# Performance work log

Measured on AMD Instinct MI355X. Metric: run time of the kernel, lower is better.

Reference implementation:

```python
import jax, jax.numpy as jnp
import numpy as np

N = 100000
E = 1600000
D = 128  # in_dim == hidden_dim


def _glorot(key, shape):
    lim = np.sqrt(6.0 / (shape[0] + shape[1]))
    return jax.random.uniform(key, shape, jnp.float32, -lim, lim)


def setup_inputs() -> dict:
    key = jax.random.key(0)
    ks = jax.random.split(key, 10)
    x = jax.random.normal(ks[0], (N, D), jnp.float32)
    edge_index = jax.random.randint(ks[1], (2, E), 0, N, jnp.int64)
    return {
        "x": x,
        "edge_index": edge_index,
        "W1": _glorot(ks[2], (D, D)), "b1": jnp.zeros((D,), jnp.float32),
        "W2": _glorot(ks[3], (D, D)), "b2": jnp.zeros((D,), jnp.float32),
        "Wv": _glorot(ks[4], (D, D)), "bv": jnp.zeros((D,), jnp.float32),
        "Wt": _glorot(ks[5], (D, D)), "bt": jnp.zeros((D,), jnp.float32),
    }


def _gcn_conv(x, W, b, src, dst, dis):
    """GCNConv: x' = D^-1/2 (A+I) D^-1/2 (x W) + b (symmetric norm, self-loops)."""
    xw = x @ W  # [N, H]
    coef = dis[src] * dis[dst]  # [E]
    msg = xw[src] * coef[:, None]  # [E, H] gathered messages
    agg = jax.ops.segment_sum(msg, dst, num_segments=x.shape[0])
    agg = agg + (dis * dis)[:, None] * xw  # self-loop contribution
    return agg + b


def reference(x, edge_index, W1, b1, W2, b2, Wv, bv, Wt, bt):
    src, dst = edge_index[0], edge_index[1]
    n = x.shape[0]
    # degree including self-loop; rsqrt normalization
    deg = jax.ops.segment_sum(jnp.ones_like(dst, dtype=x.dtype), dst, num_segments=n) + 1.0
    dis = jax.lax.rsqrt(deg)
    h = jax.nn.relu(_gcn_conv(x, W1, b1, src, dst, dis))  # dropout: eval no-op
    h = _gcn_conv(h, W2, b2, src, dst, dis)  # last layer: no relu
    x_vision = jax.nn.relu(h @ Wv + bv)
    x_text = jax.nn.relu(h @ Wt + bt)
    return (h, x_vision, x_text)
```

## Files before the change

### kernel.cpp

```cpp
#include <hip/hip_runtime.h>
#include <hip/hip_bf16.h>
#include <hip/hip_fp16.h>

#define NODES 100000
#define EDGES 1600000
#define DIM   128

typedef __bf16   bf16x8 __attribute__((ext_vector_type(8)));
typedef float    f32x4  __attribute__((ext_vector_type(4)));
typedef _Float16 f16x8  __attribute__((ext_vector_type(8)));

__device__ __forceinline__ void gather16(const void* gp, void* lp) {
    __builtin_amdgcn_global_load_lds(
        (const __attribute__((address_space(1))) void*)gp,
        (__attribute__((address_space(3))) void*)lp, 16, 0, 0);
}

__device__ __forceinline__ int wave_detect_m64(const void* ei) {
    const unsigned int* u = (const unsigned int*)ei;
    const unsigned long long nz = __ballot(u[2 * (threadIdx.x & 63) + 1] != 0);
    return (nz == 0ULL) ? 1 : 0;
}

__device__ __forceinline__ int load_idx(const void* ei, long long pos, int m64) {
    return m64 ? (int)((const long long*)ei)[pos] : ((const int*)ei)[pos];
}

__global__ __launch_bounds__(256) void init_kernel(
    int* __restrict__ deg, int n, int gn,
    const float* __restrict__ Wa, const float* __restrict__ Wb,
    const float* __restrict__ Wc, const float* __restrict__ Wd,
    __bf16* __restrict__ wfout)
{
    const int bid = blockIdx.x;
    if (bid < gn) {
        const int i = bid * 256 + threadIdx.x;
        if (i < n) deg[i] = 0;
    } else {
        const int pb = bid - gn;
        const int m  = pb >> 6;
        const int d  = (pb & 63) * 256 + threadIdx.x;
        const float* W = (m == 0) ? Wa : (m == 1) ? Wb : (m == 2) ? Wc : Wd;
        const int j  = d & 7;
        const int l  = (d >> 3) & 15;
        const int q  = (d >> 7) & 3;
        const int kt = (d >> 9) & 3;
        const int ct = (d >> 11) & 7;
        wfout[m * 16384 + d] = (__bf16)W[(kt * 32 + q * 8 + j) * DIM + ct * 16 + l];
    }
}

template <int RELU_BIAS, int ABF16, int OUTF16>
__device__ __forceinline__ void gemm_body(
    const void* __restrict__ Ain, const __bf16* __restrict__ Wf,
    const float* __restrict__ bias, void* __restrict__ outp, int M, int bid)
{
    const int wave = threadIdx.x >> 6;
    const int lane = threadIdx.x & 63;
    const int l15  = lane & 15;
    const int quad = lane >> 4;

    const int row0 = bid * 128 + wave * 32;
    if (row0 >= M) return;

    bf16x8 afA[4], afB[4];
#pragma unroll
    for (int t = 0; t < 2; t++) {
        const int arow  = row0 + t * 16 + l15;
        const int arowc = arow < M ? arow : (M - 1);
        bf16x8* af = t ? afB : afA;
        if (ABF16) {
            const __bf16* ap = (const __bf16*)Ain + (size_t)arowc * DIM + quad * 8;
#pragma unroll
            for (int kt = 0; kt < 4; kt++) af[kt] = *(const bf16x8*)(ap + kt * 32);
        } else {
            const float* ap = (const float*)Ain + (size_t)arowc * DIM + quad * 8;
#pragma unroll
            for (int kt = 0; kt < 4; kt++) {
                const f32x4 lo = *(const f32x4*)(ap + kt * 32);
                const f32x4 hi = *(const f32x4*)(ap + kt * 32 + 4);
                bf16x8 r;
#pragma unroll
                for (int j = 0; j < 4; j++) { r[j] = (__bf16)lo[j]; r[j + 4] = (__bf16)hi[j]; }
                af[kt] = r;
            }
        }
    }

#pragma unroll
    for (int ct = 0; ct < 8; ct++) {
        f32x4 cA = {0.f, 0.f, 0.f, 0.f};
        f32x4 cB = {0.f, 0.f, 0.f, 0.f};
#pragma unroll
        for (int kt = 0; kt < 4; kt++) {
            const bf16x8 b = *(const bf16x8*)(Wf + (ct * 4 + kt) * 512 + lane * 8);
            cA = __builtin_amdgcn_mfma_f32_16x16x32_bf16(afA[kt], b, cA, 0, 0, 0);
            cB = __builtin_amdgcn_mfma_f32_16x16x32_bf16(afB[kt], b, cB, 0, 0, 0);
        }
        const float bb = RELU_BIAS ? bias[ct * 16 + l15] : 0.f;
#pragma unroll
        for (int t = 0; t < 2; t++) {
            const f32x4 c = t ? cB : cA;
#pragma unroll
            for (int r = 0; r < 4; r++) {
                const int row = row0 + t * 16 + quad * 4 + r;
                if (row < M) {
                    float v = c[r];
                    if (RELU_BIAS) { v += bb; v = v > 0.f ? v : 0.f; }
                    const size_t idx = (size_t)row * DIM + ct * 16 + l15;
                    if (OUTF16) ((_Float16*)outp)[idx] = (_Float16)v;
                    else        ((float*)outp)[idx]    = v;
                }
            }
        }
    }
}

template <int RELU_BIAS, int ABF16, int OUTF16>
__global__ __launch_bounds__(256) void gemm128_kernel(
    const void* __restrict__ Ain, const __bf16* __restrict__ Wf,
    const float* __restrict__ bias, void* __restrict__ outp, int M)
{
    gemm_body<RELU_BIAS, ABF16, OUTF16>(Ain, Wf, bias, outp, M, blockIdx.x);
}

__global__ __launch_bounds__(256) void gemm1_count_kernel(
    const float* __restrict__ x, const __bf16* __restrict__ wf1,
    _Float16* __restrict__ xwh, int M, int gm,
    const void* __restrict__ ei, int* __restrict__ deg, int e_cnt)
{
    const int bid = blockIdx.x;
    if (bid < gm) {
        gemm_body<0, 0, 1>(x, wf1, nullptr, xwh, M, bid);
    } else {
        const int m64 = wave_detect_m64(ei);
        const int i = (bid - gm) * 256 + threadIdx.x;
        if (i < e_cnt) atomicAdd(&deg[load_idx(ei, (long long)EDGES + i, m64)], 1);
    }
}

__global__ __launch_bounds__(256) void gemm128_dual_kernel(
    const float* __restrict__ A,
    const __bf16* __restrict__ Wf1, const float* __restrict__ b1,
    const __bf16* __restrict__ Wf2, const float* __restrict__ b2,
    float* __restrict__ out1, float* __restrict__ out2, int M)
{
    const int wave = threadIdx.x >> 6;
    const int lane = threadIdx.x & 63;
    const int l15  = lane & 15;
    const int quad = lane >> 4;

    const int row0 = blockIdx.x * 128 + wave * 32;
    if (row0 >= M) return;

    bf16x8 afA[4], afB[4];
#pragma unroll
    for (int t = 0; t < 2; t++) {
        const int arow  = row0 + t * 16 + l15;
        const int arowc = arow < M ? arow : (M - 1);
        const float* ap = A + (size_t)arowc * DIM + quad * 8;
        bf16x8* af = t ? afB : afA;
#pragma unroll
        for (int kt = 0; kt < 4; kt++) {
            const f32x4 lo = *(const f32x4*)(ap + kt * 32);
            const f32x4 hi = *(const f32x4*)(ap + kt * 32 + 4);
            bf16x8 r;
#pragma unroll
            for (int j = 0; j < 4; j++) { r[j] = (__bf16)lo[j]; r[j + 4] = (__bf16)hi[j]; }
            af[kt] = r;
        }
    }

#pragma unroll
    for (int ct = 0; ct < 8; ct++) {
        f32x4 cA1 = {0.f,0.f,0.f,0.f}, cA2 = {0.f,0.f,0.f,0.f};
        f32x4 cB1 = {0.f,0.f,0.f,0.f}, cB2 = {0.f,0.f,0.f,0.f};
#pragma unroll
        for (int kt = 0; kt < 4; kt++) {
            const bf16x8 w1 = *(const bf16x8*)(Wf1 + (ct * 4 + kt) * 512 + lane * 8);
            const bf16x8 w2 = *(const bf16x8*)(Wf2 + (ct * 4 + kt) * 512 + lane * 8);
            cA1 = __builtin_amdgcn_mfma_f32_16x16x32_bf16(afA[kt], w1, cA1, 0, 0, 0);
            cA2 = __builtin_amdgcn_mfma_f32_16x16x32_bf16(afA[kt], w2, cA2, 0, 0, 0);
            cB1 = __builtin_amdgcn_mfma_f32_16x16x32_bf16(afB[kt], w1, cB1, 0, 0, 0);
            cB2 = __builtin_amdgcn_mfma_f32_16x16x32_bf16(afB[kt], w2, cB2, 0, 0, 0);
        }
        const float bb1 = b1[ct * 16 + l15];
        const float bb2 = b2[ct * 16 + l15];
#pragma unroll
        for (int t = 0; t < 2; t++) {
            const f32x4 c1 = t ? cB1 : cA1;
            const f32x4 c2 = t ? cB2 : cA2;
#pragma unroll
            for (int r = 0; r < 4; r++) {
                const int row = row0 + t * 16 + quad * 4 + r;
                if (row < M) {
                    float v1 = c1[r] + bb1; v1 = v1 > 0.f ? v1 : 0.f;
                    float v2 = c2[r] + bb2; v2 = v2 > 0.f ? v2 : 0.f;
                    out1[(size_t)row * DIM + ct * 16 + l15] = v1;
                    out2[(size_t)row * DIM + ct * 16 + l15] = v2;
                }
            }
        }
    }
}

__global__ __launch_bounds__(256) void scan1_kernel(const int* __restrict__ deg,
                                                    int* __restrict__ offs,
                                                    int* __restrict__ bsum,
                                                    float* __restrict__ dis, int n) {
    __shared__ int sm[256];
    const int t = threadIdx.x, i = blockIdx.x * 256 + t;
    const int v = (i < n) ? deg[i] : 0;
    sm[t] = v;
    __syncthreads();
    for (int d = 1; d < 256; d <<= 1) {
        const int add = (t >= d) ? sm[t - d] : 0;
        __syncthreads();
        sm[t] += add;
        __syncthreads();
    }
    if (i < n) {
        offs[i] = sm[t] - v;
        dis[i]  = rsqrtf((float)v + 1.0f);
    }
    if (t == 255) bsum[blockIdx.x] = sm[255];
}

__global__ __launch_bounds__(256) void scan23_kernel(int* __restrict__ offs,
                                                     const int* __restrict__ bsum,
                                                     int* __restrict__ cursor, int n) {
    __shared__ int sm[256];
    const int t = threadIdx.x, bid = blockIdx.x;
    int part = 0;
    for (int j = t; j < bid; j += 256) part += bsum[j];
    sm[t] = part;
    __syncthreads();
    for (int d = 128; d > 0; d >>= 1) {
        if (t < d) sm[t] += sm[t + d];
        __syncthreads();
    }
    const int boff = sm[0];
    const int i = bid * 256 + t;
    if (i < n) {
        const int o = offs[i] + boff;
        offs[i]   = o;
        cursor[i] = o;
    }
    if (bid == 0 && t == 0) offs[n] = EDGES;
}

__global__ __launch_bounds__(256) void fill_csr_kernel(const void* __restrict__ ei,
                                                       const float* __restrict__ dis,
                                                       int* __restrict__ cursor,
                                                       int2* __restrict__ csr,
                                                       int e_cnt) {
    const int m64 = wave_detect_m64(ei);
    const int e = blockIdx.x * 256 + threadIdx.x;
    if (e >= e_cnt) return;
    const int s = load_idx(ei, e, m64);
    const int d = load_idx(ei, (long long)EDGES + e, m64);
    const int idx = atomicAdd(&cursor[d], 1);
    int2 rec;
    rec.x = s;
    rec.y = __float_as_int(dis[s] * dis[d]);
    csr[idx] = rec;
}

template <int RELU, int WF32, int WBF16>
__global__ __launch_bounds__(256) void aggregate_kernel(
    const int* __restrict__ offs, const int2* __restrict__ csr,
    const float* __restrict__ dis, const _Float16* __restrict__ xw,
    const float* __restrict__ bias, float* __restrict__ out_f32,
    __bf16* __restrict__ out_bf, int n)
{
    __shared__ _Float16 sbuf[4][2][8 * DIM];
    const int wid  = threadIdx.x >> 6;
    const int v    = blockIdx.x * 4 + wid;
    const int lane = threadIdx.x & 63;
    const int l15  = lane & 15;
    const int seg  = lane >> 4;
    const int lmod = lane & 7;

    const int beg = offs[v];
    const int deg = offs[v + 1] - beg;
    const int nb  = (deg + 7) >> 3;
    int lim = beg + deg - 1; if (lim < 0) lim = 0;

    _Float16* bufA = &sbuf[wid][0][0];
    _Float16* bufB = &sbuf[wid][1][0];

    f32x4 a0 = {0.f,0.f,0.f,0.f}, a1 = {0.f,0.f,0.f,0.f};
    if (seg == 0) {
        const float dv = dis[v];
        const float s2 = dv * dv;
        const f16x8 xv = *(const f16x8*)(xw + (size_t)v * DIM + l15 * 8);
#pragma unroll
        for (int j = 0; j < 4; j++) {
            a0[j] += s2 * (float)xv[j];
            a1[j] += s2 * (float)xv[j + 4];
        }
    }

    int p0 = beg + lmod;            p0 = p0 < lim ? p0 : lim;
    int2 rc = csr[p0];
#pragma unroll
    for (int g = 0; g < 2; g++) {
        const int rs = __shfl(rc.x, g * 4 + seg);
        gather16(xw + (size_t)rs * DIM + l15 * 8, bufA + g * 512);
    }
    int p1 = beg + 8 + lmod;        p1 = p1 < lim ? p1 : lim;
    int2 rn1 = csr[p1];
    int p2 = beg + 16 + lmod;       p2 = p2 < lim ? p2 : lim;
    int2 rn2 = csr[p2];

    for (int b = 0; b < nb; ++b) {
        _Float16*       nbuf = (b & 1) ? bufA : bufB;
        const _Float16* cbuf = (b & 1) ? bufB : bufA;
        const bool more = (b + 1 < nb);
        int2 rn3 = rn2;

        if (more) {
#pragma unroll
            for (int g = 0; g < 2; g++) {
                const int rs = __shfl(rn1.x, g * 4 + seg);
                gather16(xw + (size_t)rs * DIM + l15 * 8, nbuf + g * 512);
            }
            __builtin_amdgcn_sched_barrier(0);
            int p3 = beg + (b + 3) * 8 + lmod;  p3 = p3 < lim ? p3 : lim;
            rn3 = csr[p3];
            __builtin_amdgcn_sched_barrier(0);
            asm volatile("s_waitcnt vmcnt(3)" ::: "memory");
            __builtin_amdgcn_sched_barrier(0);
        } else {
            asm volatile("s_waitcnt vmcnt(0)" ::: "memory");
            __builtin_amdgcn_sched_barrier(0);
        }

        const float cfy = __int_as_float(rc.y);
        const int rem = deg - b * 8;
#pragma unroll
        for (int s = 0; s < 2; s++) {
            const int r = s * 4 + seg;
            const float cr = __shfl(cfy, r);
            if (r < rem) {
                const f16x8 hv = *(const f16x8*)(cbuf + s * 512 + lane * 8);
#pragma unroll
                for (int j = 0; j < 4; j++) {
                    a0[j] += cr * (float)hv[j];
                    a1[j] += cr * (float)hv[j + 4];
                }
            }
        }
        rc = rn1; rn1 = rn2; rn2 = rn3;
    }

#pragma unroll
    for (int j = 0; j < 4; j++) {
        a0[j] += __shfl_xor(a0[j], 16); a0[j] += __shfl_xor(a0[j], 32);
        a1[j] += __shfl_xor(a1[j], 16); a1[j] += __shfl_xor(a1[j], 32);
    }

    if (seg == 0) {
        const int cc = l15 * 8;
#pragma unroll
        for (int j = 0; j < 4; j++) { a0[j] += bias[cc + j]; a1[j] += bias[cc + 4 + j]; }
        if (RELU) {
#pragma unroll
            for (int j = 0; j < 4; j++) {
                a0[j] = a0[j] > 0.f ? a0[j] : 0.f;
                a1[j] = a1[j] > 0.f ? a1[j] : 0.f;
            }
        }
        if (WF32) {
            *(f32x4*)(out_f32 + (size_t)v * DIM + cc)     = a0;
            *(f32x4*)(out_f32 + (size_t)v * DIM + cc + 4) = a1;
        }
        if (WBF16) {
            bf16x8 bv;
#pragma unroll
            for (int j = 0; j < 4; j++) { bv[j] = (__bf16)a0[j]; bv[j + 4] = (__bf16)a1[j]; }
            *(bf16x8*)(out_bf + (size_t)v * DIM + cc) = bv;
        }
    }
    asm volatile("s_waitcnt vmcnt(0)" ::: "memory");
}

extern "C" void kernel_launch(void* const* d_in, const int* in_sizes, int n_in,
                              void* d_out, int out_size, void* d_ws, size_t ws_size,
                              hipStream_t stream)
{
    const int N = NODES, E = EDGES;
    const size_t ND = (size_t)N * DIM;

    const float* x  = (const float*)d_in[0];
    const void*  ei = d_in[1];
    const float* W1 = (const float*)d_in[2];
    const float* b1 = (const float*)d_in[3];
    const float* W2 = (const float*)d_in[4];
    const float* b2 = (const float*)d_in[5];
    const float* Wv = (const float*)d_in[6];
    const float* bv = (const float*)d_in[7];
    const float* Wt = (const float*)d_in[8];
    const float* bt = (const float*)d_in[9];

    char* w = (char*)d_ws;
    int*    deg    = (int*)(w + (1 << 10));
    float*  dis    = (float*)(w + (512 << 10));
    int*    offs   = (int*)(w + (1 << 20));
    int*    cursor = (int*)(w + 1572864);
    int*    bsum   = (int*)(w + 2097152);
    int2*   csr    = (int2*)(w + 3145728);
    __bf16* wf     = (__bf16*)(w + 16000000);
    __bf16* wf1 = wf, *wf2 = wf + 16384, *wfv = wf + 32768, *wft = wf + 49152;

    float* out   = (float*)d_out;
    float* slot0 = out;
    float* slot1 = out + ND;
    float* slot2 = out + 2 * ND;
    __bf16*   h1bf = (__bf16*)slot1;
    _Float16* xwh  = (_Float16*)slot2;

    const int GN   = (N + 255) / 256;
    const int GE   = (E + 255) / 256;
    const int GM   = (N + 127) / 128;
    const int GAG  = (N + 3) / 4;

    init_kernel<<<GN + 256, 256, 0, stream>>>(deg, N, GN, W1, W2, Wv, Wt, wf);
    gemm1_count_kernel<<<GM + GE, 256, 0, stream>>>(x, wf1, xwh, N, GM, ei, deg, E);
    scan1_kernel<<<GN, 256, 0, stream>>>(deg, offs, bsum, dis, N);
    scan23_kernel<<<GN, 256, 0, stream>>>(offs, bsum, cursor, N);
    fill_csr_kernel<<<GE, 256, 0, stream>>>(ei, dis, cursor, csr, E);

    aggregate_kernel<1, 0, 1><<<GAG, 256, 0, stream>>>(offs, csr, dis, xwh, b1,
                                                       nullptr, h1bf, N);
    gemm128_kernel<0, 1, 1><<<GM, 256, 0, stream>>>(h1bf, wf2, nullptr, xwh, N);
    aggregate_kernel<0, 1, 0><<<GAG, 256, 0, stream>>>(offs, csr, dis, xwh, b2,
                                                       slot0, nullptr, N);
    gemm128_dual_kernel<<<GM, 256, 0, stream>>>(slot0, wfv, bv, wft, bt, slot1, slot2, N);
}
```

Baseline: 517.5 us.

## Build CSR with two-pass bucketed scatter instead of per-edge global atomics

Replaces the single fill_csr pass, which did one global atomic per edge on a per-node cursor, with a two-stage bucket sort. Stage A bins each chunk of 4096 edges by 128-node bucket in LDS and reserves space with one global atomic per bucket. Stage B loads each bucket's records into LDS, places them with LDS atomics and computes the coefficient. The staging buffer reuses the output slot0, and the degree zeroing now uses int4 stores. The cost is an extra kernel launch and an extra global round trip of edge records, in exchange for far fewer contended global atomics and more coalesced writes.

```diff
diff --git a/kernel.cpp b/kernel.cpp
--- a/kernel.cpp
+++ b/kernel.cpp
@@ -5,6 +5,8 @@
 #define NODES 100000
 #define EDGES 1600000
 #define DIM   128
+#define NB    782
+#define KA    4096
 
 typedef __bf16   bf16x8 __attribute__((ext_vector_type(8)));
 typedef float    f32x4  __attribute__((ext_vector_type(4)));
@@ -27,17 +29,17 @@
 }
 
 __global__ __launch_bounds__(256) void init_kernel(
-    int* __restrict__ deg, int n, int gn,
+    int* __restrict__ deg, int zcnt4, int zb,
     const float* __restrict__ Wa, const float* __restrict__ Wb,
     const float* __restrict__ Wc, const float* __restrict__ Wd,
     __bf16* __restrict__ wfout)
 {
     const int bid = blockIdx.x;
-    if (bid < gn) {
-        const int i = bid * 256 + threadIdx.x;
-        if (i < n) deg[i] = 0;
+    if (bid < zb) {
+        const int i4 = bid * 256 + threadIdx.x;
+        if (i4 < zcnt4) ((int4*)deg)[i4] = make_int4(0, 0, 0, 0);
     } else {
-        const int pb = bid - gn;
+        const int pb = bid - zb;
         const int m  = pb >> 6;
         const int d  = (pb & 63) * 256 + threadIdx.x;
         const float* W = (m == 0) ? Wa : (m == 1) ? Wb : (m == 2) ? Wc : Wd;
@@ -135,7 +137,8 @@
     } else {
         const int m64 = wave_detect_m64(ei);
         const int i = (bid - gm) * 256 + threadIdx.x;
-        if (i < e_cnt) atomicAdd(&deg[load_idx(ei, (long long)EDGES + i, m64)], 1);
+        if (i < e_cnt)
+            atomicAdd(&deg[load_idx(ei, (long long)EDGES + i, m64)], 1);
     }
 }
 
@@ -228,7 +231,7 @@
 
 __global__ __launch_bounds__(256) void scan23_kernel(int* __restrict__ offs,
                                                      const int* __restrict__ bsum,
-                                                     int* __restrict__ cursor, int n) {
+                                                     int* __restrict__ bcur, int n) {
     __shared__ int sm[256];
     const int t = threadIdx.x, bid = blockIdx.x;
     int part = 0;
@@ -243,27 +246,100 @@
     const int i = bid * 256 + t;
     if (i < n) {
         const int o = offs[i] + boff;
-        offs[i]   = o;
-        cursor[i] = o;
+        offs[i] = o;
+        if ((i & 127) == 0) bcur[i >> 7] = o;
     }
     if (bid == 0 && t == 0) offs[n] = EDGES;
 }
 
-__global__ __launch_bounds__(256) void fill_csr_kernel(const void* __restrict__ ei,
-                                                       const float* __restrict__ dis,
-                                                       int* __restrict__ cursor,
-                                                       int2* __restrict__ csr,
-                                                       int e_cnt) {
+__global__ __launch_bounds__(256) void bucketA_kernel(
+    const void* __restrict__ ei, int* __restrict__ bcur,
+    int2* __restrict__ stage, int e_cnt)
+{
+    __shared__ int2 sstage[KA];
+    __shared__ int hist[NB], lofs[NB], lcur[NB], gbase[NB];
+    __shared__ int sm[256];
     const int m64 = wave_detect_m64(ei);
-    const int e = blockIdx.x * 256 + threadIdx.x;
-    if (e >= e_cnt) return;
-    const int s = load_idx(ei, e, m64);
-    const int d = load_idx(ei, (long long)EDGES + e, m64);
-    const int idx = atomicAdd(&cursor[d], 1);
-    int2 rec;
-    rec.x = s;
-    rec.y = __float_as_int(dis[s] * dis[d]);
-    csr[idx] = rec;
+    const int t = threadIdx.x;
+    const int base = blockIdx.x * KA;
+    int cnt = e_cnt - base; cnt = cnt < KA ? cnt : KA;
+
+    for (int i = t; i < NB; i += 256) hist[i] = 0;
+    __syncthreads();
+
+    for (int j = t; j < cnt; j += 256) {
+        const int d = load_idx(ei, (long long)EDGES + base + j, m64);
+        atomicAdd(&hist[d >> 7], 1);
+    }
+    __syncthreads();
+
+    const int i0 = t * 4;
+    int h0 = (i0     < NB) ? hist[i0]     : 0;
+    int h1 = (i0 + 1 < NB) ? hist[i0 + 1] : 0;
+    int h2 = (i0 + 2 < NB) ? hist[i0 + 2] : 0;
+    int h3 = (i0 + 3 < NB) ? hist[i0 + 3] : 0;
+    const int psum = h0 + h1 + h2 + h3;
+    sm[t] = psum;
+    __syncthreads();
+    for (int d = 1; d < 256; d <<= 1) {
+        const int a = (t >= d) ? sm[t - d] : 0;
+        __syncthreads();
+        sm[t] += a;
+        __syncthreads();
+    }
+    const int ex = sm[t] - psum;
+    if (i0     < NB) { lofs[i0]     = ex;                lcur[i0]     = ex; }
+    if (i0 + 1 < NB) { lofs[i0 + 1] = ex + h0;           lcur[i0 + 1] = ex + h0; }
+    if (i0 + 2 < NB) { lofs[i0 + 2] = ex + h0 + h1;      lcur[i0 + 2] = ex + h0 + h1; }
+    if (i0 + 3 < NB) { lofs[i0 + 3] = ex + h0 + h1 + h2; lcur[i0 + 3] = ex + h0 + h1 + h2; }
+    __syncthreads();
+
+    for (int i = t; i < NB; i += 256)
+        if (hist[i] > 0) gbase[i] = atomicAdd(&bcur[i], hist[i]);
+    __syncthreads();
+
+    for (int j = t; j < cnt; j += 256) {
+        const int s = load_idx(ei, base + j, m64);
+        const int d = load_idx(ei, (long long)EDGES + base + j, m64);
+        const int p = atomicAdd(&lcur[d >> 7], 1);
+        sstage[p] = make_int2(s, d);
+    }
+    __syncthreads();
+
+    for (int j = t; j < cnt; j += 256) {
+        const int2 r = sstage[j];
+        const int b = r.y >> 7;
+        stage[gbase[b] + (j - lofs[b])] = r;
+    }
+}
+
+__global__ __launch_bounds__(256) void bucketB_kernel(
+    const int* __restrict__ offs, const float* __restrict__ dis,
+    const int2* __restrict__ stage, int2* __restrict__ csr, int n)
+{
+    __shared__ int2 recs[3072];
+    __shared__ int lcur[128];
+    const int t  = threadIdx.x;
+    const int v0 = blockIdx.x << 7;
+    int nv = n - v0; nv = nv < 128 ? nv : 128;
+    const int base = offs[v0];
+    const int cnt  = offs[v0 + nv] - base;
+    if (t < nv) lcur[t] = offs[v0 + t] - base;
+    const int lim = cnt < 3072 ? cnt : 3072;
+    for (int j = t; j < lim; j += 256) recs[j] = stage[base + j];
+    __syncthreads();
+    for (int j = t; j < lim; j += 256) {
+        const int2 r = recs[j];
+        const int pos = atomicAdd(&lcur[r.y - v0], 1);
+        const float cf = dis[r.x] * dis[r.y];
+        csr[base + pos] = make_int2(r.x, __float_as_int(cf));
+    }
+    for (int j = 3072 + t; j < cnt; j += 256) {
+        const int2 r = stage[base + j];
+        const int pos = atomicAdd(&lcur[r.y - v0], 1);
+        const float cf = dis[r.x] * dis[r.y];
+        csr[base + pos] = make_int2(r.x, __float_as_int(cf));
+    }
 }
 
 template <int RELU, int WF32, int WBF16>
@@ -404,32 +480,39 @@
     const float* bt = (const float*)d_in[9];
 
     char* w = (char*)d_ws;
-    int*    deg    = (int*)(w + (1 << 10));
-    float*  dis    = (float*)(w + (512 << 10));
-    int*    offs   = (int*)(w + (1 << 20));
-    int*    cursor = (int*)(w + 1572864);
-    int*    bsum   = (int*)(w + 2097152);
-    int2*   csr    = (int2*)(w + 3145728);
-    __bf16* wf     = (__bf16*)(w + 16000000);
+    float*  dis  = (float*)(w + 4096);
+    int*    offs = (int*)(w + 524288);
+    int*    bsum = (int*)(w + 1048576);
+    int*    bcur = (int*)(w + 1056768);
+    int*    deg  = (int*)(w + 1064960);
+    int2*   csr  = (int2*)(w + 1507328);
+    __bf16* wf   = (__bf16*)(w + 14311424);
     __bf16* wf1 = wf, *wf2 = wf + 16384, *wfv = wf + 32768, *wft = wf + 49152;
 
     float* out   = (float*)d_out;
     float* slot0 = out;
     float* slot1 = out + ND;
     float* slot2 = out + 2 * ND;
-    __bf16*   h1bf = (__bf16*)slot1;
-    _Float16* xwh  = (_Float16*)slot2;
+    __bf16*   h1bf  = (__bf16*)slot1;
+    _Float16* xwh   = (_Float16*)slot2;
+    int2*     stage = (int2*)slot0;
 
     const int GN   = (N + 255) / 256;
     const int GE   = (E + 255) / 256;
     const int GM   = (N + 127) / 128;
     const int GAG  = (N + 3) / 4;
-
-    init_kernel<<<GN + 256, 256, 0, stream>>>(deg, N, GN, W1, W2, Wv, Wt, wf);
+    const int GA   = (E + KA - 1) / KA;
+    const int GB   = NB;
+
+    const int zcnt4 = N / 4;
+    const int ZB    = (zcnt4 + 255) / 256;
+
+    init_kernel<<<ZB + 256, 256, 0, stream>>>(deg, zcnt4, ZB, W1, W2, Wv, Wt, wf);
     gemm1_count_kernel<<<GM + GE, 256, 0, stream>>>(x, wf1, xwh, N, GM, ei, deg, E);
     scan1_kernel<<<GN, 256, 0, stream>>>(deg, offs, bsum, dis, N);
-    scan23_kernel<<<GN, 256, 0, stream>>>(offs, bsum, cursor, N);
-    fill_csr_kernel<<<GE, 256, 0, stream>>>(ei, dis, cursor, csr, E);
+    scan23_kernel<<<GN, 256, 0, stream>>>(offs, bsum, bcur, N);
+    bucketA_kernel<<<GA, 256, 0, stream>>>(ei, bcur, stage, E);
+    bucketB_kernel<<<GB, 256, 0, stream>>>(offs, dis, stage, csr, N);
 
     aggregate_kernel<1, 0, 1><<<GAG, 256, 0, stream>>>(offs, csr, dis, xwh, b1,
                                                        nullptr, h1bf, N);
```

After: 487.2 us. 5.9% less time.
